# Optimization experiments

Measured on AMD Instinct MI355X. Metric: run time of the kernel, lower is better.

The kernel has to match this reference:

```python
import jax, jax.numpy as jnp
import numpy as np

E = 800000
N_NODES = 25000
NUM_RADIAL = 6
HIDDEN = 256
OUT_EMB = 256
OUT_CH = 1
NUM_LAYERS = 3


def setup_inputs() -> dict:
    key = jax.random.key(0)
    ks = jax.random.split(key, 10)
    s = lambda fan_in: 1.0 / np.sqrt(fan_in)
    return {
        "x": jax.random.normal(ks[0], (E, HIDDEN), dtype=jnp.float32),
        "rbf": jax.random.normal(ks[1], (E, NUM_RADIAL), dtype=jnp.float32),
        "i": jax.random.randint(ks[2], (E,), 0, N_NODES, dtype=jnp.int64),
        "num_nodes": N_NODES,
        "W_rbf": jax.random.normal(ks[3], (HIDDEN, NUM_RADIAL), dtype=jnp.float32) * s(NUM_RADIAL),
        "W_up": jax.random.normal(ks[4], (OUT_EMB, HIDDEN), dtype=jnp.float32) * s(HIDDEN),
        "b_up": jnp.zeros((OUT_EMB,), dtype=jnp.float32),
        "Ws": jax.random.normal(ks[5], (NUM_LAYERS, OUT_EMB, OUT_EMB), dtype=jnp.float32) * s(OUT_EMB),
        "bs": jnp.zeros((NUM_LAYERS, OUT_EMB), dtype=jnp.float32),
        "W_out": jax.random.normal(ks[6], (OUT_CH, OUT_EMB), dtype=jnp.float32) * s(OUT_EMB),
    }


def reference(x, rbf, i, num_nodes, W_rbf, W_up, b_up, Ws, bs, W_out):
    # edge-wise: lin_rbf(rbf) * x  -> [E, hidden]
    h = jnp.einsum("er,hr->eh", rbf, W_rbf) * x
    # scatter-sum edges to nodes -> [N, hidden]
    h = jax.ops.segment_sum(h, i, num_segments=num_nodes)
    # lin_up (with bias) -> [N, out_emb]
    h = jnp.einsum("nh,oh->no", h, W_up) + b_up
    # MLP stack with swish activation
    for l in range(Ws.shape[0]):
        h = jax.nn.silu(jnp.einsum("no,po->np", h, Ws[l]) + bs[l])
    # final linear, no bias -> [N, out_channels]
    return jnp.einsum("no,co->nc", h, W_out)
```

## Files before the change

### kernel.cpp

```cpp
#include <hip/hip_runtime.h>
#include <stddef.h>
#include <stdint.h>

#define E_EDGES   800000
#define N_NODES   25000
#define MROWS_PAD 25088
#define NBLK_M    196

typedef __attribute__((ext_vector_type(8))) short frag8;
typedef __attribute__((ext_vector_type(4))) float f32x4;

__device__ __forceinline__ unsigned short f2b(float f) {
    union { float f; unsigned int u; } c; c.f = f;
    unsigned int u = c.u;
    return (unsigned short)((u + 0x7fffu + ((u >> 16) & 1u)) >> 16);
}
__device__ __forceinline__ float b2f(unsigned short h) {
    union { unsigned int u; float f; } c; c.u = ((unsigned int)h) << 16;
    return c.f;
}
__device__ __forceinline__ void split2(float v, unsigned short& hi, unsigned short& lo) {
    hi = f2b(v);
    lo = f2b(v - b2f(hi));
}

__device__ __forceinline__ void gl_lds16(const void* g, void* l) {
    __builtin_amdgcn_global_load_lds(
        (const __attribute__((address_space(1))) unsigned int*)g,
        (__attribute__((address_space(3))) unsigned int*)l, 16, 0, 0);
}

__global__ void count_kernel(const int* __restrict__ idx, int* __restrict__ cnt) {
    int e = blockIdx.x * blockDim.x + threadIdx.x;
    if (e < E_EDGES) atomicAdd(&cnt[idx[e]], 1);
}

__global__ __launch_bounds__(1024) void scan_kernel(const int* __restrict__ cnt,
                                                    int* __restrict__ off,
                                                    int* __restrict__ cur) {
    __shared__ int warpsum[16];
    const int PER = 25;
    int t = threadIdx.x;
    int base = t * PER;
    int local[PER];
    int s = 0;
    #pragma unroll
    for (int j = 0; j < PER; ++j) {
        int n = base + j;
        int v = (n < N_NODES) ? cnt[n] : 0;
        local[j] = s;
        s += v;
    }
    int lane = t & 63, w = t >> 6;
    int incl = s;
    #pragma unroll
    for (int d = 1; d < 64; d <<= 1) {
        int y = __shfl_up(incl, d, 64);
        if (lane >= d) incl += y;
    }
    if (lane == 63) warpsum[w] = incl;
    __syncthreads();
    if (w == 0) {
        int v = (lane < 16) ? warpsum[lane] : 0;
        #pragma unroll
        for (int d = 1; d < 16; d <<= 1) {
            int y = __shfl_up(v, d, 64);
            if (lane >= d) v += y;
        }
        if (lane < 16) warpsum[lane] = v;
    }
    __syncthreads();
    int wbase = (w > 0) ? warpsum[w - 1] : 0;
    int texcl = wbase + (incl - s);
    #pragma unroll
    for (int j = 0; j < PER; ++j) {
        int n = base + j;
        if (n < N_NODES) { int o = texcl + local[j]; off[n] = o; cur[n] = o; }
    }
}

__global__ void fill_kernel(const int* __restrict__ idx, int* __restrict__ cur,
                            int* __restrict__ elist) {
    int e = blockIdx.x * blockDim.x + threadIdx.x;
    if (e < E_EDGES) {
        int pos = atomicAdd(&cur[idx[e]], 1);
        elist[pos] = e;
    }
}

__global__ void wconv_kernel(const float* __restrict__ Wup,
                             const float* __restrict__ Wl,
                             unsigned short* __restrict__ W2all) {
    int t = blockIdx.x * blockDim.x + threadIdx.x;
    if (t >= 4 * 65536) return;
    int m = t >> 16, rem = t & 65535;
    int o = rem >> 8, k = rem & 255;
    float v = (m == 0) ? Wup[rem] : Wl[(m - 1) * 65536 + rem];
    unsigned short hi, lo; split2(v, hi, lo);
    unsigned short* row = W2all + (size_t)m * 131072 + (size_t)o * 512;
    row[k] = hi; row[256 + k] = lo;
}

__global__ __launch_bounds__(256) void gather_kernel(
        const float* __restrict__ x, const float* __restrict__ rbf,
        const float* __restrict__ W_rbf,
        const int* __restrict__ off, const int* __restrict__ cnt,
        const int* __restrict__ elist, unsigned short* __restrict__ H2) {
    int wave = threadIdx.x >> 6;
    int lane = threadIdx.x & 63;
    int node = blockIdx.x * 4 + wave;
    if (node >= N_NODES) return;
    int c0 = lane * 4;

    float wr[4][6];
    #pragma unroll
    for (int j = 0; j < 4; ++j)
        #pragma unroll
        for (int r = 0; r < 6; ++r)
            wr[j][r] = W_rbf[(c0 + j) * 6 + r];

    float a0 = 0.f, a1 = 0.f, a2 = 0.f, a3 = 0.f;
    int start = off[node];
    int ne    = cnt[node];
    for (int base = 0; base < ne; base += 64) {
        int rem = ne - base;
        int nb  = rem < 64 ? rem : 64;
        int my_e = elist[start + base + (lane < rem ? lane : 0)];
        #pragma unroll 2
        for (int j = 0; j < nb; ++j) {
            int e = __shfl(my_e, j, 64);
            const float2* r2 = reinterpret_cast<const float2*>(rbf + (size_t)e * 6);
            float2 ra = r2[0], rb = r2[1], rc = r2[2];
            float4 xv = *reinterpret_cast<const float4*>(x + (size_t)e * 256 + c0);
            float s0 = wr[0][0]*ra.x + wr[0][1]*ra.y + wr[0][2]*rb.x + wr[0][3]*rb.y + wr[0][4]*rc.x + wr[0][5]*rc.y;
            float s1 = wr[1][0]*ra.x + wr[1][1]*ra.y + wr[1][2]*rb.x + wr[1][3]*rb.y + wr[1][4]*rc.x + wr[1][5]*rc.y;
            float s2 = wr[2][0]*ra.x + wr[2][1]*ra.y + wr[2][2]*rb.x + wr[2][3]*rb.y + wr[2][4]*rc.x + wr[2][5]*rc.y;
            float s3 = wr[3][0]*ra.x + wr[3][1]*ra.y + wr[3][2]*rb.x + wr[3][3]*rb.y + wr[3][4]*rc.x + wr[3][5]*rc.y;
            a0 += s0 * xv.x; a1 += s1 * xv.y; a2 += s2 * xv.z; a3 += s3 * xv.w;
        }
    }
    ushort4 hi4, lo4;
    split2(a0, hi4.x, lo4.x);
    split2(a1, hi4.y, lo4.y);
    split2(a2, hi4.z, lo4.z);
    split2(a3, hi4.w, lo4.w);
    *reinterpret_cast<ushort4*>(H2 + (size_t)node * 512 + c0)       = hi4;
    *reinterpret_cast<ushort4*>(H2 + (size_t)node * 512 + 256 + c0) = lo4;
}

template<int DO_SILU>
__global__ __launch_bounds__(512, 1) void gemm_mfma(
        const unsigned short* __restrict__ A2,
        const unsigned short* __restrict__ W2,
        const float* __restrict__ bias,
        unsigned short* __restrict__ C2,
        int M) {
    constexpr int NST = 12;
    __shared__ char lds[2][49152];
    int tid  = threadIdx.x;
    int row0 = blockIdx.x * 128;
    int wid  = tid >> 6, lane = tid & 63;
    int wm   = (wid >> 2) * 64;
    int wn   = (wid & 3) * 64;
    int fr   = lane & 15, fq = lane >> 4;

    f32x4 acc[4][4];
    #pragma unroll
    for (int mi = 0; mi < 4; ++mi)
        #pragma unroll
        for (int nj = 0; nj < 4; ++nj)
            acc[mi][nj] = (f32x4){0.f, 0.f, 0.f, 0.f};

    auto stage = [&](int s, int b) {
        int part = s >> 2, q = (s & 3) * 64;
        int a_k0 = (part == 2 ? 256 : 0) + q;
        int w_k0 = (part == 1 ? 256 : 0) + q;
        #pragma unroll
        for (int l = 0; l < 2; ++l) {
            int chunk = l * 512 + tid;
            int r = chunk >> 3, kc = chunk & 7;
            int kcs = kc ^ (r & 7);
            gl_lds16(A2 + (size_t)(row0 + r) * 512 + a_k0 + kcs * 8,
                     &lds[b][chunk * 16]);
        }
        #pragma unroll
        for (int l = 0; l < 4; ++l) {
            int chunk = l * 512 + tid;
            int r = chunk >> 3, kc = chunk & 7;
            int kcs = kc ^ (r & 7);
            gl_lds16(W2 + (size_t)r * 512 + w_k0 + kcs * 8,
                     &lds[b][16384 + chunk * 16]);
        }
    };

    stage(0, 0);
    __syncthreads();
    for (int s = 0; s < NST; ++s) {
        if (s + 1 < NST) stage(s + 1, (s + 1) & 1);
        const char* bufA = lds[s & 1];
        const char* bufW = lds[s & 1] + 16384;
        #pragma unroll
        for (int ks = 0; ks < 2; ++ks) {
            frag8 a[4], b[4];
            #pragma unroll
            for (int mi = 0; mi < 4; ++mi) {
                int r  = wm + mi * 16 + fr;
                int kc = ks * 4 + fq;
                int kcs = kc ^ (r & 7);
                a[mi] = *reinterpret_cast<const frag8*>(bufA + r * 128 + kcs * 16);
            }
            #pragma unroll
            for (int nj = 0; nj < 4; ++nj) {
                int r  = wn + nj * 16 + fr;
                int kc = ks * 4 + fq;
                int kcs = kc ^ (r & 7);
                b[nj] = *reinterpret_cast<const frag8*>(bufW + r * 128 + kcs * 16);
            }
            #pragma unroll
            for (int mi = 0; mi < 4; ++mi)
                #pragma unroll
                for (int nj = 0; nj < 4; ++nj)
                    acc[mi][nj] = __builtin_amdgcn_mfma_f32_16x16x32_bf16(
                        a[mi], b[nj], acc[mi][nj], 0, 0, 0);
        }
        __syncthreads();
    }

    #pragma unroll
    for (int mi = 0; mi < 4; ++mi) {
        #pragma unroll
        for (int r = 0; r < 4; ++r) {
            int grow = row0 + wm + mi * 16 + fq * 4 + r;
            if (grow < M) {
                #pragma unroll
                for (int nj = 0; nj < 4; ++nj) {
                    int col = wn + nj * 16 + fr;
                    float v = acc[mi][nj][r] + bias[col];
                    if (DO_SILU) v = v / (1.f + expf(-v));
                    unsigned short hi, lo; split2(v, hi, lo);
                    C2[(size_t)grow * 512 + col]       = hi;
                    C2[(size_t)grow * 512 + 256 + col] = lo;
                }
            }
        }
    }
}

__global__ __launch_bounds__(256) void final_kernel(const unsigned short* __restrict__ H2,
                                                    const float* __restrict__ Wout,
                                                    float* __restrict__ out, int M) {
    int wave = threadIdx.x >> 6, lane = threadIdx.x & 63;
    int row = blockIdx.x * 4 + wave;
    if (row >= M) return;
    float4 w = *reinterpret_cast<const float4*>(Wout + lane * 4);
    ushort4 h = *reinterpret_cast<const ushort4*>(H2 + (size_t)row * 512 + lane * 4);
    ushort4 l = *reinterpret_cast<const ushort4*>(H2 + (size_t)row * 512 + 256 + lane * 4);
    float s = (b2f(h.x) + b2f(l.x)) * w.x + (b2f(h.y) + b2f(l.y)) * w.y +
              (b2f(h.z) + b2f(l.z)) * w.z + (b2f(h.w) + b2f(l.w)) * w.w;
    #pragma unroll
    for (int d = 32; d > 0; d >>= 1) s += __shfl_down(s, d, 64);
    if (lane == 0) out[row] = s;
}

extern "C" void kernel_launch(void* const* d_in, const int* in_sizes, int n_in,
                              void* d_out, int out_size, void* d_ws, size_t ws_size,
                              hipStream_t stream) {
    const float* x     = (const float*)d_in[0];
    const float* rbf   = (const float*)d_in[1];
    const int*   idx   = (const int*)d_in[2];
    const float* W_rbf = (const float*)d_in[4];
    const float* W_up  = (const float*)d_in[5];
    const float* b_up  = (const float*)d_in[6];
    const float* Wl    = (const float*)d_in[7];
    const float* bl    = (const float*)d_in[8];
    const float* W_out = (const float*)d_in[9];
    float* out = (float*)d_out;

    char* ws = (char*)d_ws;
    int*            cnt   = (int*)(ws);
    int*            off   = (int*)(ws + 131072);
    int*            cur   = (int*)(ws + 262144);
    int*            elist = (int*)(ws + 393216);
    unsigned short* W2all = (unsigned short*)(ws + 3670016);
    unsigned short* H2    = (unsigned short*)(ws + 4718592);
    unsigned short* bufA2 = (unsigned short*)(ws + 30408704);
    unsigned short* bufB2 = (unsigned short*)(ws + 56098816);

    hipMemsetAsync(cnt, 0, N_NODES * sizeof(int), stream);
    count_kernel<<<(E_EDGES + 255) / 256, 256, 0, stream>>>(idx, cnt);
    scan_kernel<<<1, 1024, 0, stream>>>(cnt, off, cur);
    fill_kernel<<<(E_EDGES + 255) / 256, 256, 0, stream>>>(idx, cur, elist);
    wconv_kernel<<<1024, 256, 0, stream>>>(W_up, Wl, W2all);
    gather_kernel<<<N_NODES / 4, 256, 0, stream>>>(x, rbf, W_rbf, off, cnt, elist, H2);

    gemm_mfma<0><<<NBLK_M, 512, 0, stream>>>(H2,    W2all + 0 * 131072, b_up,     bufA2, N_NODES);
    gemm_mfma<1><<<NBLK_M, 512, 0, stream>>>(bufA2, W2all + 1 * 131072, bl + 0,   bufB2, N_NODES);
    gemm_mfma<1><<<NBLK_M, 512, 0, stream>>>(bufB2, W2all + 2 * 131072, bl + 256, bufA2, N_NODES);
    gemm_mfma<1><<<NBLK_M, 512, 0, stream>>>(bufA2, W2all + 3 * 131072, bl + 512, bufB2, N_NODES);
    final_kernel<<<(N_NODES + 3) / 4, 256, 0, stream>>>(bufB2, W_out, out, N_NODES);
}
```

Before: 1.315 ms.

## Fuse MLP stack and output projection into one LDS-resident kernel

Replaces the four separate split-bf16 GEMM launches and the final reduction kernel with one kernel. It keeps each 128-row tile of activations in LDS as fp32 across all layers, reads weights directly from global memory, and folds W_out into the last layer's epilogue. The gather kernel now writes fp32 node features (one wave per node, batched x loads, rbf loaded once per lane and shuffled), and padded rows are zeroed. This removes the intermediate HBM round-trips and launch overheads. In exchange, weight fragments are no longer staged through LDS, hi/lo splitting is redone every layer, and occupancy is limited by the 128KB LDS footprint.

After: 1.296 ms. No clear change (-1.4%).

```diff
diff --git a/kernel.cpp b/kernel.cpp
--- a/kernel.cpp
+++ b/kernel.cpp
@@ -19,9 +19,10 @@
     union { unsigned int u; float f; } c; c.u = ((unsigned int)h) << 16;
     return c.f;
 }
-__device__ __forceinline__ void split2(float v, unsigned short& hi, unsigned short& lo) {
-    hi = f2b(v);
-    lo = f2b(v - b2f(hi));
+__device__ __forceinline__ void split2(float v, short& hi, short& lo) {
+    unsigned short h = f2b(v);
+    hi = (short)h;
+    lo = (short)f2b(v - b2f(h));
 }
 
 __device__ __forceinline__ void gl_lds16(const void* g, void* l) {
@@ -96,22 +97,24 @@
     int m = t >> 16, rem = t & 65535;
     int o = rem >> 8, k = rem & 255;
     float v = (m == 0) ? Wup[rem] : Wl[(m - 1) * 65536 + rem];
-    unsigned short hi, lo; split2(v, hi, lo);
+    short hi, lo; split2(v, hi, lo);
     unsigned short* row = W2all + (size_t)m * 131072 + (size_t)o * 512;
-    row[k] = hi; row[256 + k] = lo;
-}
-
-__global__ __launch_bounds__(256) void gather_kernel(
+    row[k] = (unsigned short)hi; row[256 + k] = (unsigned short)lo;
+}
+
+__global__ __launch_bounds__(64) void gather_kernel(
         const float* __restrict__ x, const float* __restrict__ rbf,
         const float* __restrict__ W_rbf,
         const int* __restrict__ off, const int* __restrict__ cnt,
-        const int* __restrict__ elist, unsigned short* __restrict__ H2) {
-    int wave = threadIdx.x >> 6;
-    int lane = threadIdx.x & 63;
-    int node = blockIdx.x * 4 + wave;
-    if (node >= N_NODES) return;
+        const int* __restrict__ elist, float* __restrict__ node_h) {
+    int node = blockIdx.x;
+    int lane = threadIdx.x;
     int c0 = lane * 4;
-
+    float4 zero = make_float4(0.f, 0.f, 0.f, 0.f);
+    if (node >= N_NODES) {
+        *reinterpret_cast<float4*>(node_h + (size_t)node * 256 + c0) = zero;
+        return;
+    }
     float wr[4][6];
     #pragma unroll
     for (int j = 0; j < 4; ++j)
@@ -122,41 +125,56 @@
     float a0 = 0.f, a1 = 0.f, a2 = 0.f, a3 = 0.f;
     int start = off[node];
     int ne    = cnt[node];
+
     for (int base = 0; base < ne; base += 64) {
-        int rem = ne - base;
-        int nb  = rem < 64 ? rem : 64;
-        int my_e = elist[start + base + (lane < rem ? lane : 0)];
-        #pragma unroll 2
-        for (int j = 0; j < nb; ++j) {
-            int e = __shfl(my_e, j, 64);
-            const float2* r2 = reinterpret_cast<const float2*>(rbf + (size_t)e * 6);
-            float2 ra = r2[0], rb = r2[1], rc = r2[2];
-            float4 xv = *reinterpret_cast<const float4*>(x + (size_t)e * 256 + c0);
-            float s0 = wr[0][0]*ra.x + wr[0][1]*ra.y + wr[0][2]*rb.x + wr[0][3]*rb.y + wr[0][4]*rc.x + wr[0][5]*rc.y;
-            float s1 = wr[1][0]*ra.x + wr[1][1]*ra.y + wr[1][2]*rb.x + wr[1][3]*rb.y + wr[1][4]*rc.x + wr[1][5]*rc.y;
-            float s2 = wr[2][0]*ra.x + wr[2][1]*ra.y + wr[2][2]*rb.x + wr[2][3]*rb.y + wr[2][4]*rc.x + wr[2][5]*rc.y;
-            float s3 = wr[3][0]*ra.x + wr[3][1]*ra.y + wr[3][2]*rb.x + wr[3][3]*rb.y + wr[3][4]*rc.x + wr[3][5]*rc.y;
+        int nb = ne - base; if (nb > 64) nb = 64;
+        int my_e = elist[start + base + (lane < nb ? lane : nb - 1)];
+        const float* rp = rbf + (size_t)my_e * 6;
+        float2 q0 = *reinterpret_cast<const float2*>(rp);
+        float2 q1 = *reinterpret_cast<const float2*>(rp + 2);
+        float2 q2 = *reinterpret_cast<const float2*>(rp + 4);
+
+        auto edge = [&](int j, const float4& xv) {
+            float r0 = __shfl(q0.x, j, 64), r1 = __shfl(q0.y, j, 64);
+            float r2 = __shfl(q1.x, j, 64), r3 = __shfl(q1.y, j, 64);
+            float r4 = __shfl(q2.x, j, 64), r5 = __shfl(q2.y, j, 64);
+            float s0 = wr[0][0]*r0 + wr[0][1]*r1 + wr[0][2]*r2 + wr[0][3]*r3 + wr[0][4]*r4 + wr[0][5]*r5;
+            float s1 = wr[1][0]*r0 + wr[1][1]*r1 + wr[1][2]*r2 + wr[1][3]*r3 + wr[1][4]*r4 + wr[1][5]*r5;
+            float s2 = wr[2][0]*r0 + wr[2][1]*r1 + wr[2][2]*r2 + wr[2][3]*r3 + wr[2][4]*r4 + wr[2][5]*r5;
+            float s3 = wr[3][0]*r0 + wr[3][1]*r1 + wr[3][2]*r2 + wr[3][3]*r3 + wr[3][4]*r4 + wr[3][5]*r5;
             a0 += s0 * xv.x; a1 += s1 * xv.y; a2 += s2 * xv.z; a3 += s3 * xv.w;
-        }
-    }
-    ushort4 hi4, lo4;
-    split2(a0, hi4.x, lo4.x);
-    split2(a1, hi4.y, lo4.y);
-    split2(a2, hi4.z, lo4.z);
-    split2(a3, hi4.w, lo4.w);
-    *reinterpret_cast<ushort4*>(H2 + (size_t)node * 512 + c0)       = hi4;
-    *reinterpret_cast<ushort4*>(H2 + (size_t)node * 512 + 256 + c0) = lo4;
-}
-
-template<int DO_SILU>
-__global__ __launch_bounds__(512, 1) void gemm_mfma(
-        const unsigned short* __restrict__ A2,
-        const unsigned short* __restrict__ W2,
-        const float* __restrict__ bias,
-        unsigned short* __restrict__ C2,
-        int M) {
-    constexpr int NST = 12;
-    __shared__ char lds[2][49152];
+        };
+
+        int jj = 0;
+        for (; jj + 4 <= nb; jj += 4) {
+            int e0 = __shfl(my_e, jj,     64);
+            int e1 = __shfl(my_e, jj + 1, 64);
+            int e2 = __shfl(my_e, jj + 2, 64);
+            int e3 = __shfl(my_e, jj + 3, 64);
+            float4 x0 = *reinterpret_cast<const float4*>(x + (size_t)e0 * 256 + c0);
+            float4 x1 = *reinterpret_cast<const float4*>(x + (size_t)e1 * 256 + c0);
+            float4 x2 = *reinterpret_cast<const float4*>(x + (size_t)e2 * 256 + c0);
+            float4 x3 = *reinterpret_cast<const float4*>(x + (size_t)e3 * 256 + c0);
+            edge(jj, x0); edge(jj + 1, x1); edge(jj + 2, x2); edge(jj + 3, x3);
+        }
+        for (; jj < nb; ++jj) {
+            int e0 = __shfl(my_e, jj, 64);
+            float4 x0 = *reinterpret_cast<const float4*>(x + (size_t)e0 * 256 + c0);
+            edge(jj, x0);
+        }
+    }
+    *reinterpret_cast<float4*>(node_h + (size_t)node * 256 + c0) = make_float4(a0, a1, a2, a3);
+}
+
+__global__ __launch_bounds__(512, 1) void mlp_fused(
+        const float* __restrict__ node_h,
+        const unsigned short* __restrict__ W2all,
+        const float* __restrict__ b_up,
+        const float* __restrict__ bl,
+        const float* __restrict__ W_out,
+        float* __restrict__ out, int M) {
+    __shared__ float Abuf[32768];
+    __shared__ float outred[128];
     int tid  = threadIdx.x;
     int row0 = blockIdx.x * 128;
     int wid  = tid >> 6, lane = tid & 63;
@@ -164,102 +182,113 @@
     int wn   = (wid & 3) * 64;
     int fr   = lane & 15, fq = lane >> 4;
 
-    f32x4 acc[4][4];
-    #pragma unroll
-    for (int mi = 0; mi < 4; ++mi)
+    #pragma unroll
+    for (int l = 0; l < 16; ++l) {
+        int chunk = l * 512 + tid;
+        int r = chunk >> 6, u = chunk & 63;
+        int us = u ^ (r & 7);
+        gl_lds16(node_h + (size_t)(row0 + r) * 256 + us * 4,
+                 ((char*)Abuf) + (size_t)chunk * 16);
+    }
+    if (tid < 128) outred[tid] = 0.f;
+    __syncthreads();
+
+    for (int g = 0; g < 4; ++g) {
+        const unsigned short* W2 = W2all + (size_t)g * 131072;
+        const float* bias = (g == 0) ? b_up : (bl + (g - 1) * 256);
+
+        f32x4 acc[4][4];
         #pragma unroll
-        for (int nj = 0; nj < 4; ++nj)
-            acc[mi][nj] = (f32x4){0.f, 0.f, 0.f, 0.f};
-
-    auto stage = [&](int s, int b) {
-        int part = s >> 2, q = (s & 3) * 64;
-        int a_k0 = (part == 2 ? 256 : 0) + q;
-        int w_k0 = (part == 1 ? 256 : 0) + q;
+        for (int mi = 0; mi < 4; ++mi)
+            #pragma unroll
+            for (int nj = 0; nj < 4; ++nj)
+                acc[mi][nj] = (f32x4){0.f, 0.f, 0.f, 0.f};
+
         #pragma unroll
-        for (int l = 0; l < 2; ++l) {
-            int chunk = l * 512 + tid;
-            int r = chunk >> 3, kc = chunk & 7;
-            int kcs = kc ^ (r & 7);
-            gl_lds16(A2 + (size_t)(row0 + r) * 512 + a_k0 + kcs * 8,
-                     &lds[b][chunk * 16]);
-        }
-        #pragma unroll
-        for (int l = 0; l < 4; ++l) {
-            int chunk = l * 512 + tid;
-            int r = chunk >> 3, kc = chunk & 7;
-            int kcs = kc ^ (r & 7);
-            gl_lds16(W2 + (size_t)r * 512 + w_k0 + kcs * 8,
-                     &lds[b][16384 + chunk * 16]);
-        }
-    };
-
-    stage(0, 0);
-    __syncthreads();
-    for (int s = 0; s < NST; ++s) {
-        if (s + 1 < NST) stage(s + 1, (s + 1) & 1);
-        const char* bufA = lds[s & 1];
-        const char* bufW = lds[s & 1] + 16384;
-        #pragma unroll
-        for (int ks = 0; ks < 2; ++ks) {
-            frag8 a[4], b[4];
+        for (int ks = 0; ks < 8; ++ks) {
+            frag8 wh[4], wl_[4];
+            #pragma unroll
+            for (int nj = 0; nj < 4; ++nj) {
+                int wrow = wn + nj * 16 + fr;
+                const unsigned short* p = W2 + (size_t)wrow * 512 + ks * 32 + fq * 8;
+                wh[nj]  = *reinterpret_cast<const frag8*>(p);
+                wl_[nj] = *reinterpret_cast<const frag8*>(p + 256);
+            }
+            frag8 ah[4], al[4];
             #pragma unroll
             for (int mi = 0; mi < 4; ++mi) {
                 int r  = wm + mi * 16 + fr;
-                int kc = ks * 4 + fq;
-                int kcs = kc ^ (r & 7);
-                a[mi] = *reinterpret_cast<const frag8*>(bufA + r * 128 + kcs * 16);
+                int u0 = ks * 8 + fq * 2;
+                const float4 f0 = *reinterpret_cast<const float4*>(
+                    Abuf + ((size_t)r * 64 + (u0 ^ (r & 7))) * 4);
+                const float4 f1 = *reinterpret_cast<const float4*>(
+                    Abuf + ((size_t)r * 64 + ((u0 + 1) ^ (r & 7))) * 4);
+                float fv[8] = {f0.x, f0.y, f0.z, f0.w, f1.x, f1.y, f1.z, f1.w};
+                #pragma unroll
+                for (int j = 0; j < 8; ++j) {
+                    short h, l; split2(fv[j], h, l);
+                    ah[mi][j] = h; al[mi][j] = l;
+                }
             }
             #pragma unroll
-            for (int nj = 0; nj < 4; ++nj) {
-                int r  = wn + nj * 16 + fr;
-                int kc = ks * 4 + fq;
-                int kcs = kc ^ (r & 7);
-                b[nj] = *reinterpret_cast<const frag8*>(bufW + r * 128 + kcs * 16);
-            }
+            for (int mi = 0; mi < 4; ++mi)
+                #pragma unroll
+                for (int nj = 0; nj < 4; ++nj) {
+                    acc[mi][nj] = __builtin_amdgcn_mfma_f32_16x16x32_bf16(ah[mi], wh[nj],  acc[mi][nj], 0, 0, 0);
+                    acc[mi][nj] = __builtin_amdgcn_mfma_f32_16x16x32_bf16(ah[mi], wl_[nj], acc[mi][nj], 0, 0, 0);
+                    acc[mi][nj] = __builtin_amdgcn_mfma_f32_16x16x32_bf16(al[mi], wh[nj],  acc[mi][nj], 0, 0, 0);
+                }
+        }
+        __syncthreads();
+
+        if (g < 3) {
+            float bcol[4];
+            #pragma unroll
+            for (int nj = 0; nj < 4; ++nj) bcol[nj] = bias[wn + nj * 16 + fr];
             #pragma unroll
             for (int mi = 0; mi < 4; ++mi)
                 #pragma unroll
                 for (int nj = 0; nj < 4; ++nj)
-                    acc[mi][nj] = __builtin_amdgcn_mfma_f32_16x16x32_bf16(
-                        a[mi], b[nj], acc[mi][nj], 0, 0, 0);
-        }
-        __syncthreads();
-    }
-
-    #pragma unroll
-    for (int mi = 0; mi < 4; ++mi) {
-        #pragma unroll
-        for (int r = 0; r < 4; ++r) {
-            int grow = row0 + wm + mi * 16 + fq * 4 + r;
-            if (grow < M) {
+                    #pragma unroll
+                    for (int rr = 0; rr < 4; ++rr) {
+                        float v = acc[mi][nj][rr] + bcol[nj];
+                        if (g > 0) v = v / (1.f + expf(-v));
+                        int row = wm + mi * 16 + fq * 4 + rr;
+                        int col = wn + nj * 16 + fr;
+                        Abuf[((size_t)row * 64 + ((col >> 2) ^ (row & 7))) * 4 + (col & 3)] = v;
+                    }
+            __syncthreads();
+        } else {
+            float bcol[4], wo[4];
+            #pragma unroll
+            for (int nj = 0; nj < 4; ++nj) {
+                int col = wn + nj * 16 + fr;
+                bcol[nj] = bias[col]; wo[nj] = W_out[col];
+            }
+            #pragma unroll
+            for (int mi = 0; mi < 4; ++mi)
                 #pragma unroll
-                for (int nj = 0; nj < 4; ++nj) {
-                    int col = wn + nj * 16 + fr;
-                    float v = acc[mi][nj][r] + bias[col];
-                    if (DO_SILU) v = v / (1.f + expf(-v));
-                    unsigned short hi, lo; split2(v, hi, lo);
-                    C2[(size_t)grow * 512 + col]       = hi;
-                    C2[(size_t)grow * 512 + 256 + col] = lo;
+                for (int rr = 0; rr < 4; ++rr) {
+                    float p = 0.f;
+                    #pragma unroll
+                    for (int nj = 0; nj < 4; ++nj) {
+                        float v = acc[mi][nj][rr] + bcol[nj];
+                        v = v / (1.f + expf(-v));
+                        p += v * wo[nj];
+                    }
+                    p += __shfl_xor(p, 1, 64);
+                    p += __shfl_xor(p, 2, 64);
+                    p += __shfl_xor(p, 4, 64);
+                    p += __shfl_xor(p, 8, 64);
+                    if (fr == 0) atomicAdd(&outred[wm + mi * 16 + fq * 4 + rr], p);
                 }
+            __syncthreads();
+            if (tid < 128) {
+                int row = row0 + tid;
+                if (row < M) out[row] = outred[tid];
             }
         }
     }
-}
-
-__global__ __launch_bounds__(256) void final_kernel(const unsigned short* __restrict__ H2,
-                                                    const float* __restrict__ Wout,
-                                                    float* __restrict__ out, int M) {
-    int wave = threadIdx.x >> 6, lane = threadIdx.x & 63;
-    int row = blockIdx.x * 4 + wave;
-    if (row >= M) return;
-    float4 w = *reinterpret_cast<const float4*>(Wout + lane * 4);
-    ushort4 h = *reinterpret_cast<const ushort4*>(H2 + (size_t)row * 512 + lane * 4);
-    ushort4 l = *reinterpret_cast<const ushort4*>(H2 + (size_t)row * 512 + 256 + lane * 4);
-    float s = (b2f(h.x) + b2f(l.x)) * w.x + (b2f(h.y) + b2f(l.y)) * w.y +
-              (b2f(h.z) + b2f(l.z)) * w.z + (b2f(h.w) + b2f(l.w)) * w.w;
-    #pragma unroll
-    for (int d = 32; d > 0; d >>= 1) s += __shfl_down(s, d, 64);
-    if (lane == 0) out[row] = s;
 }
 
 extern "C" void kernel_launch(void* const* d_in, const int* in_sizes, int n_in,
@@ -277,25 +306,18 @@
     float* out = (float*)d_out;
 
     char* ws = (char*)d_ws;
-    int*            cnt   = (int*)(ws);
-    int*            off   = (int*)(ws + 131072);
-    int*            cur   = (int*)(ws + 262144);
-    int*            elist = (int*)(ws + 393216);
-    unsigned short* W2all = (unsigned short*)(ws + 3670016);
-    unsigned short* H2    = (unsigned short*)(ws + 4718592);
-    unsigned short* bufA2 = (unsigned short*)(ws + 30408704);
-    unsigned short* bufB2 = (unsigned short*)(ws + 56098816);
+    int*            cnt    = (int*)(ws);
+    int*            off    = (int*)(ws + 131072);
+    int*            cur    = (int*)(ws + 262144);
+    int*            elist  = (int*)(ws + 393216);
+    unsigned short* W2all  = (unsigned short*)(ws + 4194304);
+    float*          node_h = (float*)(ws + 8388608);
 
     hipMemsetAsync(cnt, 0, N_NODES * sizeof(int), stream);
     count_kernel<<<(E_EDGES + 255) / 256, 256, 0, stream>>>(idx, cnt);
     scan_kernel<<<1, 1024, 0, stream>>>(cnt, off, cur);
     fill_kernel<<<(E_EDGES + 255) / 256, 256, 0, stream>>>(idx, cur, elist);
     wconv_kernel<<<1024, 256, 0, stream>>>(W_up, Wl, W2all);
-    gather_kernel<<<N_NODES / 4, 256, 0, stream>>>(x, rbf, W_rbf, off, cnt, elist, H2);
-
-    gemm_mfma<0><<<NBLK_M, 512, 0, stream>>>(H2,    W2all + 0 * 131072, b_up,     bufA2, N_NODES);
-    gemm_mfma<1><<<NBLK_M, 512, 0, stream>>>(bufA2, W2all + 1 * 131072, bl + 0,   bufB2, N_NODES);
-    gemm_mfma<1><<<NBLK_M, 512, 0, stream>>>(bufB2, W2all + 2 * 131072, bl + 256, bufA2, N_NODES);
-    gemm_mfma<1><<<NBLK_M, 512, 0, stream>>>(bufA2, W2all + 3 * 131072, bl + 512, bufB2, N_NODES);
-    final_kernel<<<(N_NODES + 3) / 4, 256, 0, stream>>>(bufB2, W_out, out, N_NODES);
-}
+    gather_kernel<<<MROWS_PAD, 64, 0, stream>>>(x, rbf, W_rbf, off, cnt, elist, node_h);
+    mlp_fused<<<NBLK_M, 512, 0, stream>>>(node_h, W2all, b_up, bl, W_out, out, N_NODES);
+}
```
